# Kernel tuning notes

Hardware: AMD Instinct MI355X
Metric: run time of the kernel (lower is better)

Reference implementation:

```python
import jax, jax.numpy as jnp
import numpy as np
from jax import lax

B, C, HQ, WQ = 16, 256, 64, 64
HK = WK = 32
HEADS = 4
MAX_KV = 16
EPS = 1e-5  # BatchNorm2d default eps
HEAD_DIM = C // HEADS


def _bn(y, p):
    # p: [4, C] = (gamma, beta, running_mean, running_var); inference-mode BN
    g, b, m, v = p[0], p[1], p[2], p[3]
    return (y - m[:, None, None]) * (g / jnp.sqrt(v + EPS))[:, None, None] + b[:, None, None]


def _conv1x1_bn(x, w, p):
    # w: [O, C]; 1x1 conv (no bias) + BN, act=Identity
    return _bn(jnp.einsum('bchw,oc->bohw', x, w), p)


def _dwconv3x3_bn(x, w, p):
    # w: [C, 1, 3, 3] depthwise (groups=C), pad 'same'
    y = lax.conv_general_dilated(x, w, (1, 1), 'SAME', feature_group_count=C,
                                 dimension_numbers=('NCHW', 'OIHW', 'NCHW'))
    return _bn(y, p)


def _split_heads(x):
    b, c, h, w = x.shape
    return x.reshape(b, HEADS, c // HEADS, h * w).transpose(0, 1, 3, 2)  # b,heads,n,hd


def _merge_heads(x, h, w):
    b = x.shape[0]
    return x.transpose(0, 1, 3, 2).reshape(b, C, h, w)


def _pool2(x):
    # adaptive_avg_pool2d 32->16 with even ratio == exact 2x2 mean pooling
    b, c, h, w = x.shape
    return x.reshape(b, c, MAX_KV, 2, MAX_KV, 2).mean(axis=(3, 5))


def setup_inputs() -> dict:
    key = jax.random.key(0)
    ks = jax.random.split(key, 16)
    def bn_params(k):
        k1, k2, k3, k4 = jax.random.split(k, 4)
        gamma = 1.0 + 0.1 * jax.random.normal(k1, (C,), jnp.float32)
        beta = 0.1 * jax.random.normal(k2, (C,), jnp.float32)
        mean = 0.1 * jax.random.normal(k3, (C,), jnp.float32)
        var = jax.random.uniform(k4, (C,), jnp.float32, 0.5, 1.5)
        return jnp.stack([gamma, beta, mean, var])
    s = 1.0 / np.sqrt(C)
    inp = {
        'q': jax.random.normal(ks[0], (B, C, HQ, WQ), jnp.float32),
        'k': jax.random.normal(ks[1], (B, C, HK, WK), jnp.float32),
        'v': jax.random.normal(ks[2], (B, C, HK, WK), jnp.float32),
        'wq_w': s * jax.random.normal(ks[3], (C, C), jnp.float32),
        'wq_bn': bn_params(ks[4]),
        'wk_w': s * jax.random.normal(ks[5], (C, C), jnp.float32),
        'wk_bn': bn_params(ks[6]),
        'wv_w': s * jax.random.normal(ks[7], (C, C), jnp.float32),
        'wv_bn': bn_params(ks[8]),
        'pe_w': (1.0 / 3.0) * jax.random.normal(ks[9], (C, 1, 3, 3), jnp.float32),
        'pe_bn': bn_params(ks[10]),
        'proj_w': s * jax.random.normal(ks[11], (C, C), jnp.float32),
        'proj_bn': bn_params(ks[12]),
    }
    return inp


def reference(q, k, v, wq_w, wq_bn, wk_w, wk_bn, wv_w, wv_bn, pe_w, pe_bn, proj_w, proj_bn):
    # KV bounding: 32x32 > 16 -> pool to 16x16
    k = _pool2(k)
    v = _pool2(v)
    q_proj = _conv1x1_bn(q, wq_w, wq_bn)            # [B,C,64,64]
    q_s = _split_heads(q_proj)                      # [B,H,4096,64]
    k_s = _split_heads(_conv1x1_bn(k, wk_w, wk_bn)) # [B,H,256,64]
    v_s = _split_heads(_conv1x1_bn(v, wv_w, wv_bn)) # [B,H,256,64]
    scale = HEAD_DIM ** (-0.5)
    attn = jnp.einsum('bhnd,bhmd->bhnm', q_s, k_s) * scale  # [B,H,4096,256]
    attn = jax.nn.softmax(attn, axis=-1)
    y = jnp.einsum('bhnm,bhmd->bhnd', attn, v_s)    # [B,H,4096,64]
    y = _merge_heads(y, HQ, WQ) + _dwconv3x3_bn(q_proj, pe_w, pe_bn)
    return _conv1x1_bn(y, proj_w, proj_bn)
```

## Files before the change

### kernel.cpp

```cpp
#include <hip/hip_runtime.h>
#include <stdint.h>

using bf16x8 = __attribute__((ext_vector_type(8))) short;
using f32x4  = __attribute__((ext_vector_type(4))) float;
using u32x4  = __attribute__((ext_vector_type(4))) unsigned int;
using u32x2  = __attribute__((ext_vector_type(2))) unsigned int;

#define DEVFN static __device__ __forceinline__
#define MFMA16 __builtin_amdgcn_mfma_f32_16x16x32_bf16

#define NB 16
#define NC 256
#define NQ 4096

#define OFF_WQ   0u
#define OFF_WK   131072u
#define OFF_WV   262144u
#define OFF_WP   393216u
#define OFF_BQ   524288u
#define OFF_BK   525312u
#define OFF_BV   526336u
#define OFF_BP   527360u
#define OFF_PEW  528384u
#define OFF_PEB  537600u
#define OFF_QP   1048576u
#define OFF_KS   34603008u
#define OFF_VT   36700160u
#define OFF_Y    38797312u

DEVFN unsigned short f2bf(float f) {
  unsigned u = __builtin_bit_cast(unsigned, f);
  return (unsigned short)((u + 0x8000u) >> 16);
}
DEVFN float bf2f(unsigned short s) {
  return __builtin_bit_cast(float, ((unsigned)s) << 16);
}
DEVFN unsigned pk2(float a, float b) {
  return (unsigned)f2bf(a) | ((unsigned)f2bf(b) << 16);
}

union U16B { u32x4 v; unsigned u[4]; unsigned short s[8]; };

DEVFN bf16x8 ldsfrag(const u32x4* xs, int row, int kb) {
  return __builtin_bit_cast(bf16x8, xs[row * 32 + (kb ^ (row & 7))]);
}
DEVFN bf16x8 gfrag(const u32x4* w, int row, int kb) {
  return __builtin_bit_cast(bf16x8, w[row * 32 + kb]);
}

__global__ void prep_kernel(const float* __restrict__ wq, const float* __restrict__ wqbn,
                            const float* __restrict__ wk, const float* __restrict__ wkbn,
                            const float* __restrict__ wv, const float* __restrict__ wvbn,
                            const float* __restrict__ wp, const float* __restrict__ wpbn,
                            const float* __restrict__ pe, const float* __restrict__ pebn,
                            unsigned char* __restrict__ ws) {
  const int bid = blockIdx.x, c = threadIdx.x;
  if (bid < 1024) {
    const int mat = bid >> 8, o = bid & 255;
    const float* w; const float* bn; unsigned short* wd; float* bd;
    if (mat == 0)      { w = wq; bn = wqbn; wd = (unsigned short*)(ws + OFF_WQ); bd = (float*)(ws + OFF_BQ); }
    else if (mat == 1) { w = wk; bn = wkbn; wd = (unsigned short*)(ws + OFF_WK); bd = (float*)(ws + OFF_BK); }
    else if (mat == 2) { w = wv; bn = wvbn; wd = (unsigned short*)(ws + OFF_WV); bd = (float*)(ws + OFF_BV); }
    else               { w = wp; bn = wpbn; wd = (unsigned short*)(ws + OFF_WP); bd = (float*)(ws + OFF_BP); }
    const float s = bn[o] / sqrtf(bn[768 + o] + 1e-5f);
    wd[o * 256 + c] = f2bf(w[o * 256 + c] * s);
    if (c == 0) bd[o] = bn[256 + o] - bn[512 + o] * s;
  } else {
    const float s = pebn[c] / sqrtf(pebn[768 + c] + 1e-5f);
    float* pw = (float*)(ws + OFF_PEW);
    #pragma unroll
    for (int kk = 0; kk < 9; ++kk) pw[kk * 256 + c] = pe[c * 9 + kk] * s;
    ((float*)(ws + OFF_PEB))[c] = pebn[256 + c] - pebn[512 + c] * s;
  }
}

__global__ __launch_bounds__(512) void qproj_kernel(const float* __restrict__ q,
                                                    unsigned char* __restrict__ ws) {
  __shared__ u32x4 xs[4096];
  const int b = blockIdx.x >> 5, ntile = blockIdx.x & 31;
  const int t = threadIdx.x;
  {
    const int n4 = t & 31, cg = t >> 5;
    const float* qb = q + (size_t)b * NC * NQ + ntile * 128 + n4 * 4;
    f32x4 f4[16];
    #pragma unroll
    for (int cc = 0; cc < 16; ++cc)
      f4[cc] = *(const f32x4*)(qb + (size_t)(cg * 16 + cc) * NQ);
    #pragma unroll
    for (int rr = 0; rr < 4; ++rr) {
      const int row = n4 * 4 + rr;
      #pragma unroll
      for (int s = 0; s < 2; ++s) {
        U16B pk;
        #pragma unroll
        for (int j = 0; j < 8; ++j) pk.s[j] = f2bf(f4[s * 8 + j][rr]);
        xs[row * 32 + ((cg * 2 + s) ^ (row & 7))] = pk.v;
      }
    }
  }
  __syncthreads();
  const int l = t & 63, w = t >> 6;
  const int lm = l & 15, lg = l >> 4;
  const int nsub = (w & 1) * 64, osub = (w >> 1) * 64;
  const u32x4* wm = (const u32x4*)(ws + OFF_WQ);
  const f32x4 fz = {0.f, 0.f, 0.f, 0.f};
  f32x4 acc[4][4];
  #pragma unroll
  for (int i = 0; i < 4; ++i)
    #pragma unroll
    for (int j = 0; j < 4; ++j) acc[i][j] = fz;
  for (int c0 = 0; c0 < 256; c0 += 32) {
    const int kb = (c0 >> 3) + lg;
    bf16x8 af[4], bfv[4];
    #pragma unroll
    for (int i = 0; i < 4; ++i) af[i] = gfrag(wm, osub + i * 16 + lm, kb);
    #pragma unroll
    for (int j = 0; j < 4; ++j) bfv[j] = ldsfrag(xs, nsub + j * 16 + lm, kb);
    #pragma unroll
    for (int i = 0; i < 4; ++i)
      #pragma unroll
      for (int j = 0; j < 4; ++j) acc[i][j] = MFMA16(af[i], bfv[j], acc[i][j], 0, 0, 0);
  }
  const float* bias = (const float*)(ws + OFF_BQ);
  unsigned short* qp = (unsigned short*)(ws + OFF_QP) + ((size_t)b * NQ + ntile * 128) * NC;
  #pragma unroll
  for (int i = 0; i < 4; ++i) {
    const int ob = osub + i * 16 + lg * 4;
    const f32x4 b4 = *(const f32x4*)(bias + ob);
    #pragma unroll
    for (int j = 0; j < 4; ++j) {
      const int n = nsub + j * 16 + lm;
      u32x2 pv = { pk2(acc[i][j][0] + b4[0], acc[i][j][1] + b4[1]),
                   pk2(acc[i][j][2] + b4[2], acc[i][j][3] + b4[3]) };
      *(u32x2*)(qp + (size_t)n * NC + ob) = pv;
    }
  }
}

__global__ __launch_bounds__(512) void kvproj_kernel(const float* __restrict__ kin,
                                                     const float* __restrict__ vin,
                                                     unsigned char* __restrict__ ws) {
  __shared__ u32x4 xs[1024];
  const int bid = blockIdx.x;
  const int b = bid >> 4, which = (bid >> 3) & 1, part = bid & 7;
  const int t = threadIdx.x;
  {
    const int nl = t & 31, cq = t >> 5;
    const int kv = part * 32 + nl;
    const int yy = kv >> 4, xx = kv & 15;
    const float* src = (which ? vin : kin) + (size_t)b * NC * 1024 + (2 * yy) * 32 + 2 * xx;
    #pragma unroll
    for (int s = 0; s < 2; ++s) {
      const int c0 = cq * 16 + s * 8;
      U16B pk;
      #pragma unroll
      for (int j = 0; j < 8; ++j) {
        const float* p = src + (size_t)(c0 + j) * 1024;
        const float2 p01 = *(const float2*)p;
        const float2 p23 = *(const float2*)(p + 32);
        pk.s[j] = f2bf((p01.x + p01.y + p23.x + p23.y) * 0.25f);
      }
      xs[nl * 32 + ((c0 >> 3) ^ (nl & 7))] = pk.v;
    }
  }
  __syncthreads();
  const int l = t & 63, w = t >> 6;
  const int lm = l & 15, lg = l >> 4;
  const int osub = (w >> 1) * 64;
  const int kvsub = (w & 1) * 16;
  const f32x4 fz = {0.f, 0.f, 0.f, 0.f};
  if (which == 0) {
    const u32x4* wm = (const u32x4*)(ws + OFF_WK);
    f32x4 acc[4];
    #pragma unroll
    for (int i = 0; i < 4; ++i) acc[i] = fz;
    for (int c0 = 0; c0 < 256; c0 += 32) {
      const int kb = (c0 >> 3) + lg;
      bf16x8 bfv = ldsfrag(xs, kvsub + lm, kb);
      #pragma unroll
      for (int i = 0; i < 4; ++i) {
        bf16x8 af = gfrag(wm, osub + i * 16 + lm, kb);
        acc[i] = MFMA16(af, bfv, acc[i], 0, 0, 0);
      }
    }
    const float* bias = (const float*)(ws + OFF_BK);
    unsigned short* ksd = (unsigned short*)(ws + OFF_KS) + (size_t)b * 256 * NC;
    const int kv = part * 32 + kvsub + lm;
    #pragma unroll
    for (int i = 0; i < 4; ++i) {
      const int ob = osub + i * 16 + lg * 4;
      const f32x4 b4 = *(const f32x4*)(bias + ob);
      u32x2 pv = { pk2(acc[i][0] + b4[0], acc[i][1] + b4[1]),
                   pk2(acc[i][2] + b4[2], acc[i][3] + b4[3]) };
      *(u32x2*)(ksd + (size_t)kv * NC + ob) = pv;
    }
  } else {
    const u32x4* wm = (const u32x4*)(ws + OFF_WV);
    f32x4 acc[4];
    #pragma unroll
    for (int j = 0; j < 4; ++j) acc[j] = fz;
    for (int c0 = 0; c0 < 256; c0 += 32) {
      const int kb = (c0 >> 3) + lg;
      bf16x8 af = ldsfrag(xs, kvsub + lm, kb);
      #pragma unroll
      for (int j = 0; j < 4; ++j) {
        bf16x8 bfv = gfrag(wm, osub + j * 16 + lm, kb);
        acc[j] = MFMA16(af, bfv, acc[j], 0, 0, 0);
      }
    }
    const float* bias = (const float*)(ws + OFF_BV);
    unsigned short* vtd = (unsigned short*)(ws + OFF_VT) + (size_t)b * 256 * 256;
    const int kvb = part * 32 + kvsub + lg * 4;
    #pragma unroll
    for (int j = 0; j < 4; ++j) {
      const int o = osub + j * 16 + lm;
      const float bo = bias[o];
      u32x2 pv = { pk2(acc[j][0] + bo, acc[j][1] + bo),
                   pk2(acc[j][2] + bo, acc[j][3] + bo) };
      *(u32x2*)(vtd + (size_t)o * 256 + kvb) = pv;
    }
  }
}

__global__ __launch_bounds__(256) void attn_kernel(unsigned char* __restrict__ ws) {
  __shared__ u32x4 plds[2048];
  __shared__ float sums[4][16];
  const int bid = blockIdx.x;
  const int qt = bid & 63, h = (bid >> 6) & 3, b = bid >> 8;
  const int t = threadIdx.x, w = t >> 6, l = t & 63;
  const int lm = l & 15, lg = l >> 4;
  const int q0 = qt * 64 + w * 16;
  const u32x4* qp = (const u32x4*)(ws + OFF_QP) + (size_t)b * NQ * 32;
  const u32x4* ksp = (const u32x4*)(ws + OFF_KS) + (size_t)b * 256 * 32;
  const u32x4* vtp = (const u32x4*)(ws + OFF_VT) + (size_t)(b * 4 + h) * 64 * 32;

  bf16x8 qf[2];
  #pragma unroll
  for (int kk = 0; kk < 2; ++kk)
    qf[kk] = __builtin_bit_cast(bf16x8, qp[(q0 + lm) * 32 + h * 8 + kk * 4 + lg]);

  const f32x4 fz = {0.f, 0.f, 0.f, 0.f};
  f32x4 st[16];
  #pragma unroll
  for (int tk = 0; tk < 16; ++tk) st[tk] = fz;
  #pragma unroll
  for (int tk = 0; tk < 16; ++tk) {
    #pragma unroll
    for (int kk = 0; kk < 2; ++kk) {
      bf16x8 kf = __builtin_bit_cast(bf16x8, ksp[(tk * 16 + lm) * 32 + h * 8 + kk * 4 + lg]);
      st[tk] = MFMA16(kf, qf[kk], st[tk], 0, 0, 0);
    }
  }
  float mx = -3.0e38f;
  #pragma unroll
  for (int tk = 0; tk < 16; ++tk)
    #pragma unroll
    for (int r = 0; r < 4; ++r) mx = fmaxf(mx, st[tk][r]);
  mx = fmaxf(mx, __shfl_xor(mx, 16));
  mx = fmaxf(mx, __shfl_xor(mx, 32));
  float sum = 0.f;
  #pragma unroll
  for (int tk = 0; tk < 16; ++tk)
    #pragma unroll
    for (int r = 0; r < 4; ++r) {
      const float e = __expf(0.125f * (st[tk][r] - mx));
      st[tk][r] = e; sum += e;
    }
  sum += __shfl_xor(sum, 16);
  sum += __shfl_xor(sum, 32);
  if (l < 16) sums[w][l] = sum;
  u32x2* pw = (u32x2*)(plds + w * 512);
  #pragma unroll
  for (int tk = 0; tk < 16; ++tk) {
    const int slot = (2 * tk + (lg >> 1)) ^ (lm & 7);
    u32x2 pv = { pk2(st[tk][0], st[tk][1]), pk2(st[tk][2], st[tk][3]) };
    pw[lm * 64 + slot * 2 + (lg & 1)] = pv;
  }
  __syncthreads();
  f32x4 yacc[4];
  #pragma unroll
  for (int jj = 0; jj < 4; ++jj) yacc[jj] = fz;
  const u32x4* pr = plds + w * 512;
  for (int kk = 0; kk < 8; ++kk) {
    bf16x8 pf = __builtin_bit_cast(bf16x8, pr[lm * 32 + ((kk * 4 + lg) ^ (lm & 7))]);
    #pragma unroll
    for (int jj = 0; jj < 4; ++jj) {
      bf16x8 vf = __builtin_bit_cast(bf16x8, vtp[(jj * 16 + lm) * 32 + kk * 4 + lg]);
      yacc[jj] = MFMA16(pf, vf, yacc[jj], 0, 0, 0);
    }
  }
  unsigned short* yo = (unsigned short*)(ws + OFF_Y) + (size_t)b * NQ * NC;
  #pragma unroll
  for (int r = 0; r < 4; ++r) {
    const float inv = __builtin_amdgcn_rcpf(sums[w][lg * 4 + r]);
    const size_t rowoff = (size_t)(q0 + lg * 4 + r) * NC + h * 64;
    #pragma unroll
    for (int jj = 0; jj < 4; ++jj)
      yo[rowoff + jj * 16 + lm] = f2bf(yacc[jj][r] * inv);
  }
}

__global__ __launch_bounds__(512) void final_kernel(float* __restrict__ out,
                                                    unsigned char* __restrict__ ws) {
  __shared__ u32x4 xs[4096];
  const int b = blockIdx.x >> 5, ntile = blockIdx.x & 31;
  const int t = threadIdx.x;
  {
    const int nl = t & 127, cq = t >> 7;
    const int n = ntile * 128 + nl;
    const int yy = n >> 6, xx = n & 63;
    const u32x4* qp = (const u32x4*)(ws + OFF_QP) + (size_t)b * NQ * 32;
    const u32x4* yv = (const u32x4*)(ws + OFF_Y) + (size_t)b * NQ * 32;
    const float* pew = (const float*)(ws + OFF_PEW);
    const float* peb = (const float*)(ws + OFF_PEB);
    #pragma unroll
    for (int it = 0; it < 8; ++it) {
      const int c0 = cq * 8 + it * 32, cb = c0 >> 3;
      float a8[8];
      #pragma unroll
      for (int j = 0; j < 8; ++j) a8[j] = peb[c0 + j];
      #pragma unroll
      for (int dy = -1; dy <= 1; ++dy) {
        #pragma unroll
        for (int dx = -1; dx <= 1; ++dx) {
          const int y2 = yy + dy, x2 = xx + dx;
          if (y2 >= 0 && y2 < 64 && x2 >= 0 && x2 < 64) {
            U16B qv; qv.v = qp[(size_t)(y2 * 64 + x2) * 32 + cb];
            const float* wr = pew + ((dy + 1) * 3 + (dx + 1)) * 256 + c0;
            #pragma unroll
            for (int j = 0; j < 8; ++j) a8[j] += bf2f(qv.s[j]) * wr[j];
          }
        }
      }
      U16B yvv; yvv.v = yv[(size_t)n * 32 + cb];
      U16B pk;
      #pragma unroll
      for (int j = 0; j < 8; ++j) pk.s[j] = f2bf(a8[j] + bf2f(yvv.s[j]));
      xs[nl * 32 + (cb ^ (nl & 7))] = pk.v;
    }
  }
  __syncthreads();
  const int l = t & 63, w = t >> 6;
  const int lm = l & 15, lg = l >> 4;
  const int osub = (w >> 1) * 64, nsub = (w & 1) * 64;
  const u32x4* wm = (const u32x4*)(ws + OFF_WP);
  const f32x4 fz = {0.f, 0.f, 0.f, 0.f};
  f32x4 acc[4][4];
  #pragma unroll
  for (int i = 0; i < 4; ++i)
    #pragma unroll
    for (int j = 0; j < 4; ++j) acc[i][j] = fz;
  for (int c0 = 0; c0 < 256; c0 += 32) {
    const int kb = (c0 >> 3) + lg;
    bf16x8 af[4], bfv[4];
    #pragma unroll
    for (int i = 0; i < 4; ++i) af[i] = ldsfrag(xs, nsub + i * 16 + lm, kb);
    #pragma unroll
    for (int j = 0; j < 4; ++j) bfv[j] = gfrag(wm, osub + j * 16 + lm, kb);
    #pragma unroll
    for (int i = 0; i < 4; ++i)
      #pragma unroll
      for (int j = 0; j < 4; ++j) acc[i][j] = MFMA16(af[i], bfv[j], acc[i][j], 0, 0, 0);
  }
  const float* bias = (const float*)(ws + OFF_BP);
  float* ob = out + (size_t)b * NC * NQ + ntile * 128;
  #pragma unroll
  for (int j = 0; j < 4; ++j) {
    const int o = osub + j * 16 + lm;
    const float bo = bias[o];
    #pragma unroll
    for (int i = 0; i < 4; ++i) {
      const int nb = nsub + i * 16 + lg * 4;
      f32x4 v = { acc[i][j][0] + bo, acc[i][j][1] + bo, acc[i][j][2] + bo, acc[i][j][3] + bo };
      *(f32x4*)(ob + (size_t)o * NQ + nb) = v;
    }
  }
}

extern "C" void kernel_launch(void* const* d_in, const int* in_sizes, int n_in,
                              void* d_out, int out_size, void* d_ws, size_t ws_size,
                              hipStream_t stream) {
  const float* q    = (const float*)d_in[0];
  const float* k    = (const float*)d_in[1];
  const float* v    = (const float*)d_in[2];
  const float* wq   = (const float*)d_in[3];
  const float* wqbn = (const float*)d_in[4];
  const float* wk   = (const float*)d_in[5];
  const float* wkbn = (const float*)d_in[6];
  const float* wv   = (const float*)d_in[7];
  const float* wvbn = (const float*)d_in[8];
  const float* pe   = (const float*)d_in[9];
  const float* pebn = (const float*)d_in[10];
  const float* wp   = (const float*)d_in[11];
  const float* wpbn = (const float*)d_in[12];
  unsigned char* ws = (unsigned char*)d_ws;

  prep_kernel<<<1025, 256, 0, stream>>>(wq, wqbn, wk, wkbn, wv, wvbn, wp, wpbn, pe, pebn, ws);
  qproj_kernel<<<512, 512, 0, stream>>>(q, ws);
  kvproj_kernel<<<256, 512, 0, stream>>>(k, v, ws);
  attn_kernel<<<4096, 256, 0, stream>>>(ws);
  final_kernel<<<512, 512, 0, stream>>>((float*)d_out, ws);
}
```

Baseline: 423.9 us.

## Switch attention to 32x32 MFMA with register-resident P, dropping LDS round-trip

The attention kernel now uses 32x32x16 bf16 MFMA tiles with each wave handling 32 queries, so a block covers 128 queries and the grid is halved. The softmax probabilities stay in registers and are fed straight to the PV MFMA as the B operand. This removes the LDS staging, the swizzle and the __syncthreads. To make that register layout line up, the V-transpose writer in kvproj permutes its kv row groups. Register pressure rises (8 f32x16 score tiles per thread), which may lower occupancy.

```diff
diff --git a/kernel.cpp b/kernel.cpp
--- a/kernel.cpp
+++ b/kernel.cpp
@@ -3,11 +3,13 @@
 
 using bf16x8 = __attribute__((ext_vector_type(8))) short;
 using f32x4  = __attribute__((ext_vector_type(4))) float;
+using f32x16 = __attribute__((ext_vector_type(16))) float;
 using u32x4  = __attribute__((ext_vector_type(4))) unsigned int;
 using u32x2  = __attribute__((ext_vector_type(2))) unsigned int;
 
 #define DEVFN static __device__ __forceinline__
 #define MFMA16 __builtin_amdgcn_mfma_f32_16x16x32_bf16
+#define MFMA32 __builtin_amdgcn_mfma_f32_32x32x16_bf16
 
 #define NB 16
 #define NC 256
@@ -210,7 +212,8 @@
     }
     const float* bias = (const float*)(ws + OFF_BV);
     unsigned short* vtd = (unsigned short*)(ws + OFF_VT) + (size_t)b * 256 * 256;
-    const int kvb = part * 32 + kvsub + lg * 4;
+    const int gp = ((lg & 1) << 1) | (lg >> 1);
+    const int kvb = part * 32 + kvsub + gp * 4;
     #pragma unroll
     for (int j = 0; j < 4; ++j) {
       const int o = osub + j * 16 + lm;
@@ -223,80 +226,97 @@
 }
 
 __global__ __launch_bounds__(256) void attn_kernel(unsigned char* __restrict__ ws) {
-  __shared__ u32x4 plds[2048];
-  __shared__ float sums[4][16];
   const int bid = blockIdx.x;
-  const int qt = bid & 63, h = (bid >> 6) & 3, b = bid >> 8;
+  const int qt = bid & 31, h = (bid >> 5) & 3, b = bid >> 7;
   const int t = threadIdx.x, w = t >> 6, l = t & 63;
-  const int lm = l & 15, lg = l >> 4;
-  const int q0 = qt * 64 + w * 16;
-  const u32x4* qp = (const u32x4*)(ws + OFF_QP) + (size_t)b * NQ * 32;
+  const int ql = l & 31, hi = l >> 5;
+  const int q0 = qt * 128 + w * 32;
+  const u32x4* qp  = (const u32x4*)(ws + OFF_QP) + (size_t)b * NQ * 32;
   const u32x4* ksp = (const u32x4*)(ws + OFF_KS) + (size_t)b * 256 * 32;
   const u32x4* vtp = (const u32x4*)(ws + OFF_VT) + (size_t)(b * 4 + h) * 64 * 32;
 
-  bf16x8 qf[2];
-  #pragma unroll
-  for (int kk = 0; kk < 2; ++kk)
-    qf[kk] = __builtin_bit_cast(bf16x8, qp[(q0 + lm) * 32 + h * 8 + kk * 4 + lg]);
-
-  const f32x4 fz = {0.f, 0.f, 0.f, 0.f};
-  f32x4 st[16];
-  #pragma unroll
-  for (int tk = 0; tk < 16; ++tk) st[tk] = fz;
-  #pragma unroll
-  for (int tk = 0; tk < 16; ++tk) {
-    #pragma unroll
-    for (int kk = 0; kk < 2; ++kk) {
-      bf16x8 kf = __builtin_bit_cast(bf16x8, ksp[(tk * 16 + lm) * 32 + h * 8 + kk * 4 + lg]);
-      st[tk] = MFMA16(kf, qf[kk], st[tk], 0, 0, 0);
-    }
-  }
-  float mx = -3.0e38f;
-  #pragma unroll
-  for (int tk = 0; tk < 16; ++tk)
-    #pragma unroll
-    for (int r = 0; r < 4; ++r) mx = fmaxf(mx, st[tk][r]);
-  mx = fmaxf(mx, __shfl_xor(mx, 16));
+  bf16x8 qf[4];
+  #pragma unroll
+  for (int c = 0; c < 4; ++c)
+    qf[c] = __builtin_bit_cast(bf16x8, qp[(size_t)(q0 + ql) * 32 + h * 8 + 2 * c + hi]);
+
+  f32x16 st[8];
+  #pragma unroll
+  for (int tt = 0; tt < 8; ++tt)
+    #pragma unroll
+    for (int r = 0; r < 16; ++r) st[tt][r] = 0.f;
+
+  #pragma unroll
+  for (int tt = 0; tt < 8; ++tt) {
+    #pragma unroll
+    for (int c = 0; c < 4; ++c) {
+      bf16x8 kf = __builtin_bit_cast(bf16x8, ksp[(size_t)(tt * 32 + ql) * 32 + h * 8 + 2 * c + hi]);
+      st[tt] = MFMA32(kf, qf[c], st[tt], 0, 0, 0);
+    }
+  }
+
+  f32x16 mv;
+  #pragma unroll
+  for (int r = 0; r < 16; ++r) {
+    float m0 = fmaxf(fmaxf(st[0][r], st[1][r]), fmaxf(st[2][r], st[3][r]));
+    float m1 = fmaxf(fmaxf(st[4][r], st[5][r]), fmaxf(st[6][r], st[7][r]));
+    mv[r] = fmaxf(m0, m1);
+  }
+  float mx = mv[0];
+  #pragma unroll
+  for (int r = 1; r < 16; ++r) mx = fmaxf(mx, mv[r]);
   mx = fmaxf(mx, __shfl_xor(mx, 32));
+
+  f32x16 ev;
+  #pragma unroll
+  for (int r = 0; r < 16; ++r) ev[r] = 0.f;
+  #pragma unroll
+  for (int tt = 0; tt < 8; ++tt) {
+    #pragma unroll
+    for (int r = 0; r < 16; ++r) {
+      const float e = __expf(0.125f * (st[tt][r] - mx));
+      st[tt][r] = e;
+      ev[r] += e;
+    }
+  }
   float sum = 0.f;
   #pragma unroll
-  for (int tk = 0; tk < 16; ++tk)
-    #pragma unroll
-    for (int r = 0; r < 4; ++r) {
-      const float e = __expf(0.125f * (st[tk][r] - mx));
-      st[tk][r] = e; sum += e;
-    }
-  sum += __shfl_xor(sum, 16);
+  for (int r = 0; r < 16; ++r) sum += ev[r];
   sum += __shfl_xor(sum, 32);
-  if (l < 16) sums[w][l] = sum;
-  u32x2* pw = (u32x2*)(plds + w * 512);
-  #pragma unroll
-  for (int tk = 0; tk < 16; ++tk) {
-    const int slot = (2 * tk + (lg >> 1)) ^ (lm & 7);
-    u32x2 pv = { pk2(st[tk][0], st[tk][1]), pk2(st[tk][2], st[tk][3]) };
-    pw[lm * 64 + slot * 2 + (lg & 1)] = pv;
-  }
-  __syncthreads();
-  f32x4 yacc[4];
-  #pragma unroll
-  for (int jj = 0; jj < 4; ++jj) yacc[jj] = fz;
-  const u32x4* pr = plds + w * 512;
-  for (int kk = 0; kk < 8; ++kk) {
-    bf16x8 pf = __builtin_bit_cast(bf16x8, pr[lm * 32 + ((kk * 4 + lg) ^ (lm & 7))]);
-    #pragma unroll
-    for (int jj = 0; jj < 4; ++jj) {
-      bf16x8 vf = __builtin_bit_cast(bf16x8, vtp[(jj * 16 + lm) * 32 + kk * 4 + lg]);
-      yacc[jj] = MFMA16(pf, vf, yacc[jj], 0, 0, 0);
-    }
-  }
-  unsigned short* yo = (unsigned short*)(ws + OFF_Y) + (size_t)b * NQ * NC;
-  #pragma unroll
-  for (int r = 0; r < 4; ++r) {
-    const float inv = __builtin_amdgcn_rcpf(sums[w][lg * 4 + r]);
-    const size_t rowoff = (size_t)(q0 + lg * 4 + r) * NC + h * 64;
-    #pragma unroll
-    for (int jj = 0; jj < 4; ++jj)
-      yo[rowoff + jj * 16 + lm] = f2bf(yacc[jj][r] * inv);
+  const float inv = __builtin_amdgcn_rcpf(sum);
+
+  f32x16 yacc[2];
+  #pragma unroll
+  for (int jj = 0; jj < 2; ++jj)
+    #pragma unroll
+    for (int r = 0; r < 16; ++r) yacc[jj][r] = 0.f;
+
+  #pragma unroll
+  for (int step = 0; step < 16; ++step) {
+    const int tt = step >> 1, bse = 8 * (step & 1);
+    U16B pb;
+    pb.u[0] = pk2(st[tt][bse + 0], st[tt][bse + 1]);
+    pb.u[1] = pk2(st[tt][bse + 2], st[tt][bse + 3]);
+    pb.u[2] = pk2(st[tt][bse + 4], st[tt][bse + 5]);
+    pb.u[3] = pk2(st[tt][bse + 6], st[tt][bse + 7]);
+    const bf16x8 pa = __builtin_bit_cast(bf16x8, pb.v);
+    #pragma unroll
+    for (int jj = 0; jj < 2; ++jj) {
+      bf16x8 vf = __builtin_bit_cast(bf16x8, vtp[(size_t)(jj * 32 + ql) * 32 + step * 2 + hi]);
+      yacc[jj] = MFMA32(vf, pa, yacc[jj], 0, 0, 0);
+    }
+  }
+
+  unsigned short* yo = (unsigned short*)(ws + OFF_Y) + ((size_t)b * NQ + q0 + ql) * NC + h * 64;
+  #pragma unroll
+  for (int jj = 0; jj < 2; ++jj) {
+    #pragma unroll
+    for (int g = 0; g < 4; ++g) {
+      const int d = 32 * jj + 8 * g + 4 * hi;
+      u32x2 pv = { pk2(yacc[jj][4 * g + 0] * inv, yacc[jj][4 * g + 1] * inv),
+                   pk2(yacc[jj][4 * g + 2] * inv, yacc[jj][4 * g + 3] * inv) };
+      *(u32x2*)(yo + d) = pv;
+    }
   }
 }
 
@@ -398,6 +418,6 @@
   prep_kernel<<<1025, 256, 0, stream>>>(wq, wqbn, wk, wkbn, wv, wvbn, wp, wpbn, pe, pebn, ws);
   qproj_kernel<<<512, 512, 0, stream>>>(q, ws);
   kvproj_kernel<<<256, 512, 0, stream>>>(k, v, ws);
-  attn_kernel<<<4096, 256, 0, stream>>>(ws);
+  attn_kernel<<<2048, 256, 0, stream>>>(ws);
   final_kernel<<<512, 512, 0, stream>>>((float*)d_out, ws);
 }
```

Measured after the change: 373.5 us. 11.9% less time.
